# Performance work log

Hardware: AMD Instinct MI355X
Metric: run time of the kernel (lower is better)

Reference implementation:

```python
import jax, jax.numpy as jnp
import numpy as np

B, T, C = 4, 2048, 1024
H, D = 16, 64  # num_heads, head_size; H*D == C


def setup_inputs() -> dict:
    key = jax.random.key(0)
    k1, k2, k3 = jax.random.split(key, 3)
    x = jax.random.normal(k1, (B, T, C), dtype=jnp.float32)
    w_qkv = jax.random.normal(k2, (C, 3 * C), dtype=jnp.float32) * (C ** -0.5)
    w_out = jax.random.normal(k3, (C, C), dtype=jnp.float32) * (C ** -0.5)
    b_out = jnp.zeros((C,), dtype=jnp.float32)
    return {"x": x, "w_qkv": w_qkv, "w_out": w_out, "b_out": b_out}


def reference(x, w_qkv, w_out, b_out):
    Bb, Tt, Cc = x.shape
    qkv = x @ w_qkv                        # [B,T,3C]
    q, k, v = jnp.split(qkv, 3, axis=2)
    # [B,T,C] -> [B,H,T,D]
    q = q.reshape(Bb, Tt, H, D).transpose(0, 2, 1, 3)
    k = k.reshape(Bb, Tt, H, D).transpose(0, 2, 1, 3)
    v = v.reshape(Bb, Tt, H, D).transpose(0, 2, 1, 3)
    scores = jnp.einsum('bhqd,bhkd->bhqk', q, k) * (D ** -0.5)
    causal = jnp.tril(jnp.ones((Tt, Tt), dtype=bool))
    scores = jnp.where(causal, scores, -jnp.inf)
    attn = jax.nn.softmax(scores, axis=-1)  # dropout is identity in eval mode
    out = jnp.einsum('bhqk,bhkd->bhqd', attn, v)
    out = out.transpose(0, 2, 1, 3).reshape(Bb, Tt, Cc)
    return out @ w_out + b_out
```

## Files before the change

### kernel.cpp

```cpp
#include <hip/hip_runtime.h>

typedef __bf16 bf16;
typedef __bf16 bf16x4 __attribute__((ext_vector_type(4)));
typedef __bf16 bf16x8 __attribute__((ext_vector_type(8)));
typedef float  f32x4  __attribute__((ext_vector_type(4)));

#define MFMA16(A_, B_, C_) __builtin_amdgcn_mfma_f32_16x16x32_bf16((A_), (B_), (C_), 0, 0, 0)

#define BB 4
#define TT 2048
#define CC 1024
#define HH 16
#define DD 64
#define MM (BB * TT)
#define N_QKV (3 * CC)
#define LDSS 72
#define BSTRIDE 36
#define QSCALE2 0.18033688f

static __device__ __forceinline__ void store_lds8(bf16* p, bf16x8 v) {
  bf16x4 lo, hi;
#pragma unroll
  for (int i = 0; i < 4; i++) { lo[i] = v[i]; hi[i] = v[i + 4]; }
  *(bf16x4*)p = lo;
  *(bf16x4*)(p + 4) = hi;
}

static __device__ __forceinline__ bf16x8 load_lds8(const bf16* p) {
  bf16x4 lo = *(const bf16x4*)p;
  bf16x4 hi = *(const bf16x4*)(p + 4);
  bf16x8 v;
#pragma unroll
  for (int i = 0; i < 4; i++) { v[i] = lo[i]; v[i + 4] = hi[i]; }
  return v;
}

static __device__ __forceinline__ void async_cp16(const bf16* g, bf16* l) {
  __builtin_amdgcn_global_load_lds(
      (const __attribute__((address_space(1))) void*)g,
      (__attribute__((address_space(3))) void*)l, 16, 0, 0);
}

__global__ __launch_bounds__(256) void sniff_k(const unsigned short* __restrict__ u,
                                               int* __restrict__ flag) {
  __shared__ int s;
  if (threadIdx.x == 0) s = 0;
  __syncthreads();
  int c = 0;
  for (int i = threadIdx.x; i < 65536; i += 256)
    if ((u[i] & 0x7F80u) == 0x7F80u) c = 1;
  if (c) atomicOr(&s, 1);
  __syncthreads();
  if (threadIdx.x == 0) *flag = s;
}

__global__ __launch_bounds__(256) void cvt_k(const void* __restrict__ in,
                                             bf16* __restrict__ out,
                                             const int* __restrict__ flag,
                                             size_t off) {
  const int fl = *flag;
  const size_t i = ((size_t)blockIdx.x * 256 + threadIdx.x) * 8;
  if (fl) {
    f32x4 a = *(const f32x4*)((const float*)in + off + i);
    f32x4 b = *(const f32x4*)((const float*)in + off + i + 4);
    bf16x8 o;
#pragma unroll
    for (int j = 0; j < 4; j++) { o[j] = (bf16)a[j]; o[4 + j] = (bf16)b[j]; }
    *(bf16x8*)(out + i) = o;
  } else {
    *(bf16x8*)(out + i) = *(const bf16x8*)((const bf16*)in + off + i);
  }
}

__global__ __launch_bounds__(256) void transpose_k(const void* __restrict__ in,
                                                   bf16* __restrict__ out,
                                                   int R, int C,
                                                   const int* __restrict__ flag) {
  __shared__ bf16 tile[32][33];
  const int fl = *flag;
  const int c0 = blockIdx.x * 32, r0 = blockIdx.y * 32;
  const int tx = threadIdx.x & 31, ty = threadIdx.x >> 5;
#pragma unroll
  for (int i = ty; i < 32; i += 8) {
    const size_t idx = (size_t)(r0 + i) * C + c0 + tx;
    tile[i][tx] = fl ? (bf16)((const float*)in)[idx] : ((const bf16*)in)[idx];
  }
  __syncthreads();
#pragma unroll
  for (int i = ty; i < 32; i += 8)
    out[(size_t)(c0 + i) * R + r0 + tx] = tile[tx][i];
}

__global__ __launch_bounds__(256) void vtrans_k(const bf16* __restrict__ qkv,
                                                bf16* __restrict__ vt) {
  __shared__ bf16 tile[32][33];
  const int bh = blockIdx.z;
  const int t0 = blockIdx.x * 32, d0 = blockIdx.y * 32;
  const bf16* src = qkv + (size_t)(bh >> 4) * TT * N_QKV + 2 * CC + (bh & 15) * DD;
  const int tx = threadIdx.x & 31, ty = threadIdx.x >> 5;
#pragma unroll
  for (int i = ty; i < 32; i += 8)
    tile[i][tx] = src[(size_t)(t0 + i) * N_QKV + d0 + tx];
  __syncthreads();
  bf16* dst = vt + ((size_t)bh * DD + d0) * TT + t0;
#pragma unroll
  for (int i = ty; i < 32; i += 8)
    dst[(size_t)i * TT + tx] = tile[tx][i];
}

template <int EPI>
__global__ __launch_bounds__(256) void gemm_lds(const bf16* __restrict__ A,
                                                const bf16* __restrict__ Bt,
                                                const void* __restrict__ biasv,
                                                void* __restrict__ Cv,
                                                const int* __restrict__ flag,
                                                size_t aoff, size_t coff,
                                                int M, int N, int K,
                                                int lda, int ldc) {
  const int fl = *flag;
  __shared__ __align__(16) bf16 sA[128 * 32];
  __shared__ __align__(16) bf16 sB[128 * 32];
  const int tid = threadIdx.x;
  const int lane = tid & 63, wave = tid >> 6;
  const int quad = lane >> 4, l15 = lane & 15;
  const int wr = wave >> 1, wc = wave & 1;
  const int m0 = blockIdx.x * 128, n0 = blockIdx.y * 128;
  const int grow = lane >> 2;
  const int gcol = (lane & 3) * 8;

  f32x4 acc[4][4];
#pragma unroll
  for (int i = 0; i < 4; i++)
#pragma unroll
    for (int j = 0; j < 4; j++) {
      f32x4 z = {0.f, 0.f, 0.f, 0.f};
      acc[i][j] = z;
    }

  const bf16* Ag = A + aoff + (size_t)(m0 + wave * 32 + grow) * lda + gcol;
  const bf16* Bg = Bt + (size_t)(n0 + wave * 32 + grow) * K + gcol;
  bf16* sAw = sA + wave * 32 * 32;
  bf16* sBw = sB + wave * 32 * 32;

  for (int k0 = 0; k0 < K; k0 += 32) {
    __syncthreads();
    async_cp16(Ag, sAw);
    async_cp16(Ag + (size_t)16 * lda, sAw + 16 * 32);
    async_cp16(Bg, sBw);
    async_cp16(Bg + (size_t)16 * K, sBw + 16 * 32);
    Ag += 32;
    Bg += 32;
    __syncthreads();

    bf16x8 af[4], bfr[4];
#pragma unroll
    for (int mi = 0; mi < 4; mi++)
      af[mi] = *(const bf16x8*)(sA + (wr * 64 + mi * 16 + l15) * 32 + quad * 8);
#pragma unroll
    for (int ni = 0; ni < 4; ni++)
      bfr[ni] = *(const bf16x8*)(sB + (wc * 64 + ni * 16 + l15) * 32 + quad * 8);
#pragma unroll
    for (int mi = 0; mi < 4; mi++)
#pragma unroll
      for (int ni = 0; ni < 4; ni++)
        acc[mi][ni] = MFMA16(af[mi], bfr[ni], acc[mi][ni]);
  }

#pragma unroll
  for (int mi = 0; mi < 4; mi++) {
#pragma unroll
    for (int r = 0; r < 4; r++) {
      const int m = m0 + wr * 64 + mi * 16 + quad * 4 + r;
#pragma unroll
      for (int ni = 0; ni < 4; ni++) {
        const int n = n0 + wc * 64 + ni * 16 + l15;
        float v = acc[mi][ni][r];
        const size_t idx = coff + (size_t)m * ldc + n;
        if (EPI == 1) {
          v += fl ? ((const float*)biasv)[n] : (float)((const bf16*)biasv)[n];
          if (fl) ((float*)Cv)[idx] = v;
          else    ((bf16*)Cv)[idx] = (bf16)v;
        } else {
          ((bf16*)Cv)[idx] = (bf16)v;
        }
      }
    }
  }
}

template <int EPI, bool AF>
__global__ __launch_bounds__(256) void gemm_bt(const void* __restrict__ Av,
                                               const bf16* __restrict__ Bt,
                                               const void* __restrict__ biasv,
                                               void* __restrict__ Cv,
                                               const int* __restrict__ flag,
                                               size_t aoff, size_t coff,
                                               int M, int N, int K,
                                               int lda, int ldc) {
  const int fl = *flag;
  const bool af32 = AF && (fl != 0);
  __shared__ __align__(16) bf16 sA[128 * 32];
  __shared__ __align__(16) bf16 sB[128 * 32];
  const int tid = threadIdx.x;
  const int lane = tid & 63, wave = tid >> 6;
  const int quad = lane >> 4, l15 = lane & 15;
  const int wr = wave >> 1, wc = wave & 1;
  const int m0 = blockIdx.x * 128, n0 = blockIdx.y * 128;
  const int srow = tid >> 2;
  const int scol = (tid & 3) * 8;

  f32x4 acc[4][4];
#pragma unroll
  for (int i = 0; i < 4; i++)
#pragma unroll
    for (int j = 0; j < 4; j++) {
      f32x4 z = {0.f, 0.f, 0.f, 0.f};
      acc[i][j] = z;
    }

  const size_t abase0 = aoff + (size_t)(m0 + srow) * lda + scol;
  const size_t abase1 = abase0 + (size_t)64 * lda;
  const bf16* Bg0 = Bt + (size_t)(n0 + srow) * K + scol;
  const bf16* Bg1 = Bg0 + (size_t)64 * K;

  for (int k0 = 0; k0 < K; k0 += 32) {
    bf16x8 a0, a1;
    if (af32) {
      const float* Af = (const float*)Av;
      f32x4 p00 = *(const f32x4*)(Af + abase0 + k0);
      f32x4 p01 = *(const f32x4*)(Af + abase0 + k0 + 4);
      f32x4 p10 = *(const f32x4*)(Af + abase1 + k0);
      f32x4 p11 = *(const f32x4*)(Af + abase1 + k0 + 4);
#pragma unroll
      for (int i = 0; i < 4; i++) {
        a0[i] = (bf16)p00[i]; a0[i + 4] = (bf16)p01[i];
        a1[i] = (bf16)p10[i]; a1[i + 4] = (bf16)p11[i];
      }
    } else {
      const bf16* Ab = (const bf16*)Av;
      a0 = *(const bf16x8*)(Ab + abase0 + k0);
      a1 = *(const bf16x8*)(Ab + abase1 + k0);
    }
    bf16x8 b0 = *(const bf16x8*)(Bg0 + k0);
    bf16x8 b1 = *(const bf16x8*)(Bg1 + k0);
    __syncthreads();
    *(bf16x8*)(sA + srow * 32 + scol) = a0;
    *(bf16x8*)(sA + (64 + srow) * 32 + scol) = a1;
    *(bf16x8*)(sB + srow * 32 + scol) = b0;
    *(bf16x8*)(sB + (64 + srow) * 32 + scol) = b1;
    __syncthreads();

    bf16x8 af[4], bfr[4];
#pragma unroll
    for (int mi = 0; mi < 4; mi++)
      af[mi] = *(const bf16x8*)(sA + (wr * 64 + mi * 16 + l15) * 32 + quad * 8);
#pragma unroll
    for (int ni = 0; ni < 4; ni++)
      bfr[ni] = *(const bf16x8*)(sB + (wc * 64 + ni * 16 + l15) * 32 + quad * 8);
#pragma unroll
    for (int mi = 0; mi < 4; mi++)
#pragma unroll
      for (int ni = 0; ni < 4; ni++)
        acc[mi][ni] = MFMA16(af[mi], bfr[ni], acc[mi][ni]);
  }

#pragma unroll
  for (int mi = 0; mi < 4; mi++) {
#pragma unroll
    for (int r = 0; r < 4; r++) {
      const int m = m0 + wr * 64 + mi * 16 + quad * 4 + r;
#pragma unroll
      for (int ni = 0; ni < 4; ni++) {
        const int n = n0 + wc * 64 + ni * 16 + l15;
        float v = acc[mi][ni][r];
        const size_t idx = coff + (size_t)m * ldc + n;
        if (EPI == 1) {
          v += fl ? ((const float*)biasv)[n] : (float)((const bf16*)biasv)[n];
          if (fl) ((float*)Cv)[idx] = v;
          else    ((bf16*)Cv)[idx] = (bf16)v;
        } else {
          ((bf16*)Cv)[idx] = (bf16)v;
        }
      }
    }
  }
}

template <int EPI, bool AF, bool WF>
__global__ __launch_bounds__(256) void gemm_nt(const void* __restrict__ Av,
                                               const void* __restrict__ Wv,
                                               const void* __restrict__ biasv,
                                               void* __restrict__ Cv,
                                               const int* __restrict__ flag,
                                               size_t aoff, size_t coff,
                                               int M, int N, int K,
                                               int lda, int ldc) {
  const int fl = *flag;
  const bool af32 = AF && (fl != 0);
  const bool wf32 = WF && (fl != 0);
  __shared__ __align__(16) bf16 sA[128 * 32];
  __shared__ __align__(16) bf16 sB[128 * BSTRIDE];
  const int tid = threadIdx.x;
  const int lane = tid & 63, wave = tid >> 6;
  const int quad = lane >> 4, l15 = lane & 15;
  const int wr = wave >> 1, wc = wave & 1;
  const int m0 = blockIdx.x * 128, n0 = blockIdx.y * 128;
  const int arow = tid >> 2, acol = (tid & 3) * 8;
  const int wk = tid >> 3, wn = (tid & 7) * 16;

  f32x4 acc[4][4];
#pragma unroll
  for (int i = 0; i < 4; i++)
#pragma unroll
    for (int j = 0; j < 4; j++) {
      f32x4 z = {0.f, 0.f, 0.f, 0.f};
      acc[i][j] = z;
    }

  const size_t abase0 = aoff + (size_t)(m0 + arow) * lda + acol;
  const size_t abase1 = abase0 + (size_t)64 * lda;

  for (int k0 = 0; k0 < K; k0 += 32) {
    bf16x8 a0, a1;
    if (af32) {
      const float* Af = (const float*)Av;
      f32x4 p00 = *(const f32x4*)(Af + abase0 + k0);
      f32x4 p01 = *(const f32x4*)(Af + abase0 + k0 + 4);
      f32x4 p10 = *(const f32x4*)(Af + abase1 + k0);
      f32x4 p11 = *(const f32x4*)(Af + abase1 + k0 + 4);
#pragma unroll
      for (int i = 0; i < 4; i++) {
        a0[i] = (bf16)p00[i]; a0[i + 4] = (bf16)p01[i];
        a1[i] = (bf16)p10[i]; a1[i + 4] = (bf16)p11[i];
      }
    } else {
      const bf16* Ab = (const bf16*)Av;
      a0 = *(const bf16x8*)(Ab + abase0 + k0);
      a1 = *(const bf16x8*)(Ab + abase1 + k0);
    }
    bf16 wreg[16];
    const size_t wbase = (size_t)(k0 + wk) * N + n0 + wn;
    if (wf32) {
      const float* Wf = (const float*)Wv;
      f32x4 q0 = *(const f32x4*)(Wf + wbase);
      f32x4 q1 = *(const f32x4*)(Wf + wbase + 4);
      f32x4 q2 = *(const f32x4*)(Wf + wbase + 8);
      f32x4 q3 = *(const f32x4*)(Wf + wbase + 12);
#pragma unroll
      for (int i = 0; i < 4; i++) {
        wreg[i] = (bf16)q0[i];      wreg[4 + i] = (bf16)q1[i];
        wreg[8 + i] = (bf16)q2[i];  wreg[12 + i] = (bf16)q3[i];
      }
    } else {
      const bf16* Wb = (const bf16*)Wv;
      bf16x8 w0 = *(const bf16x8*)(Wb + wbase);
      bf16x8 w1 = *(const bf16x8*)(Wb + wbase + 8);
#pragma unroll
      for (int i = 0; i < 8; i++) { wreg[i] = w0[i]; wreg[8 + i] = w1[i]; }
    }
    __syncthreads();
    *(bf16x8*)(sA + arow * 32 + acol) = a0;
    *(bf16x8*)(sA + (64 + arow) * 32 + acol) = a1;
#pragma unroll
    for (int i = 0; i < 16; i++)
      sB[(wn + i) * BSTRIDE + wk] = wreg[i];
    __syncthreads();

    bf16x8 af[4], bfr[4];
#pragma unroll
    for (int mi = 0; mi < 4; mi++)
      af[mi] = *(const bf16x8*)(sA + (wr * 64 + mi * 16 + l15) * 32 + quad * 8);
#pragma unroll
    for (int ni = 0; ni < 4; ni++)
      bfr[ni] = load_lds8(sB + (wc * 64 + ni * 16 + l15) * BSTRIDE + quad * 8);
#pragma unroll
    for (int mi = 0; mi < 4; mi++)
#pragma unroll
      for (int ni = 0; ni < 4; ni++)
        acc[mi][ni] = MFMA16(af[mi], bfr[ni], acc[mi][ni]);
  }

#pragma unroll
  for (int mi = 0; mi < 4; mi++) {
#pragma unroll
    for (int r = 0; r < 4; r++) {
      const int m = m0 + wr * 64 + mi * 16 + quad * 4 + r;
#pragma unroll
      for (int ni = 0; ni < 4; ni++) {
        const int n = n0 + wc * 64 + ni * 16 + l15;
        float v = acc[mi][ni][r];
        const size_t idx = coff + (size_t)m * ldc + n;
        if (EPI == 1) {
          v += fl ? ((const float*)biasv)[n] : (float)((const bf16*)biasv)[n];
          if (fl) ((float*)Cv)[idx] = v;
          else    ((bf16*)Cv)[idx] = (bf16)v;
        } else {
          ((bf16*)Cv)[idx] = (bf16)v;
        }
      }
    }
  }
}

__global__ __launch_bounds__(256) void attn_k(bf16* __restrict__ qkv,
                                              const bf16* __restrict__ vt) {
  __shared__ __align__(16) bf16 sP[128 * LDSS];
  __shared__ __align__(16) bf16 sK[64 * LDSS];
  __shared__ __align__(16) bf16 sVt[64 * LDSS];

  const int tid = threadIdx.x;
  const int lane = tid & 63, wave = tid >> 6;
  const int quad = lane >> 4, l15 = lane & 15;
  const int bh = blockIdx.x;
  bf16* base = qkv + (size_t)(bh >> 4) * TT * N_QKV + (bh & 15) * DD;
  const bf16* Qp = base;
  const bf16* Kp = base + CC;
  const bf16* vhead = vt + (size_t)bh * DD * TT;

  const int qt = 15 - (int)blockIdx.y;
  const int q0 = qt * 128;
  const int wave_row0 = q0 + wave * 32;
  bf16* sPw = sP + (size_t)(wave * 32) * LDSS;

  const int krow = tid >> 2;
  const int kcol = (tid & 3) * 16;

  bf16x8 ones;
  {
    const bf16 o = (l15 == 0) ? (bf16)1.0f : (bf16)0.0f;
#pragma unroll
    for (int i = 0; i < 8; i++) ones[i] = o;
  }

  bf16x8 aq[2][2];
#pragma unroll
  for (int mi = 0; mi < 2; mi++)
#pragma unroll
    for (int ks = 0; ks < 2; ks++) {
      bf16x8 v = *(const bf16x8*)(Qp + (size_t)(wave_row0 + mi * 16 + l15) * N_QKV +
                                  ks * 32 + quad * 8);
#pragma unroll
      for (int i = 0; i < 8; i++) v[i] = (bf16)((float)v[i] * QSCALE2);
      aq[mi][ks] = v;
    }

  bf16x8 kr0, kr1, vr0, vr1;
  {
    const bf16* kp = Kp + (size_t)krow * N_QKV + kcol;
    kr0 = *(const bf16x8*)kp;
    kr1 = *(const bf16x8*)(kp + 8);
    const bf16* vp = vhead + (size_t)krow * TT + kcol;
    vr0 = *(const bf16x8*)vp;
    vr1 = *(const bf16x8*)(vp + 8);
  }

  f32x4 Oacc[2][4];
  f32x4 lacc[2];
#pragma unroll
  for (int mi = 0; mi < 2; mi++) {
    f32x4 z = {0.f, 0.f, 0.f, 0.f};
    lacc[mi] = z;
#pragma unroll
    for (int nt = 0; nt < 4; nt++) Oacc[mi][nt] = z;
  }

  const int jmax = q0 + 64;

  for (int j0 = 0; j0 <= jmax; j0 += 64) {
    __syncthreads();
    *(bf16x8*)(sK + krow * LDSS + kcol) = kr0;
    *(bf16x8*)(sK + krow * LDSS + kcol + 8) = kr1;
    *(bf16x8*)(sVt + krow * LDSS + kcol) = vr0;
    *(bf16x8*)(sVt + krow * LDSS + kcol + 8) = vr1;
    __syncthreads();

    if (j0 + 64 <= jmax) {
      const bf16* kp = Kp + (size_t)(j0 + 64 + krow) * N_QKV + kcol;
      kr0 = *(const bf16x8*)kp;
      kr1 = *(const bf16x8*)(kp + 8);
      const bf16* vp = vhead + (size_t)krow * TT + j0 + 64 + kcol;
      vr0 = *(const bf16x8*)vp;
      vr1 = *(const bf16x8*)(vp + 8);
    }

    if (j0 <= wave_row0 + 31) {
      f32x4 S[2][4];
#pragma unroll
      for (int mi = 0; mi < 2; mi++)
#pragma unroll
        for (int kt = 0; kt < 4; kt++) {
          f32x4 z = {0.f, 0.f, 0.f, 0.f};
          S[mi][kt] = z;
        }
      __builtin_amdgcn_s_setprio(1);
#pragma unroll
      for (int kt = 0; kt < 4; kt++) {
        const bf16* kp = sK + (size_t)(kt * 16 + l15) * LDSS + quad * 8;
        bf16x8 k0 = *(const bf16x8*)kp;
        bf16x8 k1 = *(const bf16x8*)(kp + 32);
        S[0][kt] = MFMA16(k0, aq[0][0], S[0][kt]);
        S[0][kt] = MFMA16(k1, aq[0][1], S[0][kt]);
        S[1][kt] = MFMA16(k0, aq[1][0], S[1][kt]);
        S[1][kt] = MFMA16(k1, aq[1][1], S[1][kt]);
      }
      __builtin_amdgcn_s_setprio(0);

      const bool needmask = (j0 + 63 > wave_row0);
#pragma unroll
      for (int mi = 0; mi < 2; mi++) {
        const int qg = wave_row0 + mi * 16 + l15;
#pragma unroll
        for (int kt = 0; kt < 4; kt++) {
          const int kb = j0 + kt * 16 + quad * 4;
          bf16x4 pk;
#pragma unroll
          for (int r = 0; r < 4; r++) {
            float e = __builtin_amdgcn_exp2f(S[mi][kt][r]);
            if (needmask && (kb + r > qg)) e = 0.f;
            pk[r] = (bf16)e;
          }
          *(bf16x4*)(sPw + (size_t)(mi * 16 + l15) * LDSS + kt * 16 + quad * 4) = pk;
        }
      }

      bf16x8 ap0[2], ap1[2];
#pragma unroll
      for (int mi = 0; mi < 2; mi++) {
        const bf16* pp = sPw + (size_t)(mi * 16 + l15) * LDSS + quad * 8;
        ap0[mi] = *(const bf16x8*)pp;
        ap1[mi] = *(const bf16x8*)(pp + 32);
      }
      __builtin_amdgcn_s_setprio(1);
#pragma unroll
      for (int mi = 0; mi < 2; mi++) {
        lacc[mi] = MFMA16(ap0[mi], ones, lacc[mi]);
        lacc[mi] = MFMA16(ap1[mi], ones, lacc[mi]);
      }
#pragma unroll
      for (int nt = 0; nt < 4; nt++) {
        const bf16* vp = sVt + (size_t)(nt * 16 + l15) * LDSS + quad * 8;
        bf16x8 v0 = *(const bf16x8*)vp;
        bf16x8 v1 = *(const bf16x8*)(vp + 32);
        Oacc[0][nt] = MFMA16(ap0[0], v0, Oacc[0][nt]);
        Oacc[0][nt] = MFMA16(ap1[0], v1, Oacc[0][nt]);
        Oacc[1][nt] = MFMA16(ap0[1], v0, Oacc[1][nt]);
        Oacc[1][nt] = MFMA16(ap1[1], v1, Oacc[1][nt]);
      }
      __builtin_amdgcn_s_setprio(0);
    }
  }

#pragma unroll
  for (int mi = 0; mi < 2; mi++)
#pragma unroll
    for (int r = 0; r < 4; r++) {
      const float lv = __shfl(lacc[mi][r], lane & 48, 64);
      const float invl = 1.0f / lv;
      const int t = q0 + wave * 32 + mi * 16 + quad * 4 + r;
#pragma unroll
      for (int nt = 0; nt < 4; nt++)
        base[(size_t)t * N_QKV + nt * 16 + l15] =
            (bf16)(Oacc[mi][nt][r] * invl);
    }
}

__global__ __launch_bounds__(256) void attn_s(bf16* __restrict__ qkv) {
  __shared__ __align__(16) bf16 sQ[128 * LDSS];
  __shared__ __align__(16) bf16 sK[64 * LDSS];
  __shared__ __align__(16) bf16 sVt[64 * LDSS];

  const int tid = threadIdx.x;
  const int lane = tid & 63, wave = tid >> 6;
  const int quad = lane >> 4, l15 = lane & 15;
  const int bh = blockIdx.x;
  bf16* base = qkv + (size_t)(bh >> 4) * TT * N_QKV + (bh & 15) * DD;
  const bf16* Qp = base;
  const bf16* Kp = base + CC;
  const bf16* Vp = base + 2 * CC;

  const int krow = tid >> 2;
  const int kcol = (tid & 3) * 16;
  const int vkey = tid & 31;
  const int vcol = (tid >> 5) * 8;

  bf16x8 ones;
  {
    const bf16 o = (l15 == 0) ? (bf16)1.0f : (bf16)0.0f;
#pragma unroll
    for (int i = 0; i < 8; i++) ones[i] = o;
  }

  const int qt = 15 - (int)blockIdx.y;
  const int q0 = qt * 128;

#pragma unroll
  for (int p = 0; p < 2; p++) {
    const int r = p * 64 + krow;
    const bf16* src = Qp + (size_t)(q0 + r) * N_QKV + kcol;
    bf16x8 v0 = *(const bf16x8*)src;
    bf16x8 v1 = *(const bf16x8*)(src + 8);
#pragma unroll
    for (int i = 0; i < 8; i++) {
      v0[i] = (bf16)((float)v0[i] * QSCALE2);
      v1[i] = (bf16)((float)v1[i] * QSCALE2);
    }
    *(bf16x8*)(sQ + r * LDSS + kcol) = v0;
    *(bf16x8*)(sQ + r * LDSS + kcol + 8) = v1;
  }

  bf16x8 kr0, kr1, vr0, vr1;
  {
    const bf16* kp = Kp + (size_t)krow * N_QKV + kcol;
    kr0 = *(const bf16x8*)kp;
    kr1 = *(const bf16x8*)(kp + 8);
    vr0 = *(const bf16x8*)(Vp + (size_t)vkey * N_QKV + vcol);
    vr1 = *(const bf16x8*)(Vp + (size_t)(32 + vkey) * N_QKV + vcol);
  }
  __syncthreads();

  bf16x8 aq[2][2];
#pragma unroll
  for (int mi = 0; mi < 2; mi++) {
    const bf16* qp = sQ + (size_t)(wave * 32 + mi * 16 + l15) * LDSS + quad * 8;
    aq[mi][0] = *(const bf16x8*)qp;
    aq[mi][1] = *(const bf16x8*)(qp + 32);
  }

  f32x4 Oacc[2][4];
  f32x4 lacc[2];
#pragma unroll
  for (int mi = 0; mi < 2; mi++) {
    f32x4 z = {0.f, 0.f, 0.f, 0.f};
    lacc[mi] = z;
#pragma unroll
    for (int nt = 0; nt < 4; nt++) Oacc[mi][nt] = z;
  }

  const int jmax = q0 + 64;
  const int wave_row0 = q0 + wave * 32;
  bf16* sP = sQ + (size_t)(wave * 32) * LDSS;

  for (int j0 = 0; j0 <= jmax; j0 += 64) {
    __syncthreads();
    *(bf16x8*)(sK + krow * LDSS + kcol) = kr0;
    *(bf16x8*)(sK + krow * LDSS + kcol + 8) = kr1;
#pragma unroll
    for (int i = 0; i < 8; i++) {
      sVt[(vcol + i) * LDSS + vkey] = vr0[i];
      sVt[(vcol + i) * LDSS + 32 + vkey] = vr1[i];
    }
    __syncthreads();

    if (j0 + 64 <= jmax) {
      const bf16* kp = Kp + (size_t)(j0 + 64 + krow) * N_QKV + kcol;
      kr0 = *(const bf16x8*)kp;
      kr1 = *(const bf16x8*)(kp + 8);
      vr0 = *(const bf16x8*)(Vp + (size_t)(j0 + 64 + vkey) * N_QKV + vcol);
      vr1 = *(const bf16x8*)(Vp + (size_t)(j0 + 96 + vkey) * N_QKV + vcol);
    }

    if (j0 <= wave_row0 + 31) {
      f32x4 S[2][4];
#pragma unroll
      for (int nt = 0; nt < 4; nt++) {
        const bf16* kp = sK + (size_t)(nt * 16 + l15) * LDSS + quad * 8;
        bf16x8 bk0 = *(const bf16x8*)kp;
        bf16x8 bk1 = *(const bf16x8*)(kp + 32);
#pragma unroll
        for (int mi = 0; mi < 2; mi++) {
          f32x4 acc = {0.f, 0.f, 0.f, 0.f};
          acc = MFMA16(aq[mi][0], bk0, acc);
          acc = MFMA16(aq[mi][1], bk1, acc);
          S[mi][nt] = acc;
        }
      }

      const bool needmask = (j0 + 63 > wave_row0);
#pragma unroll
      for (int mi = 0; mi < 2; mi++)
#pragma unroll
        for (int nt = 0; nt < 4; nt++) {
          const int kc = j0 + nt * 16 + l15;
#pragma unroll
          for (int r = 0; r < 4; r++) {
            float e = __builtin_amdgcn_exp2f(S[mi][nt][r]);
            if (needmask && kc > wave_row0 + mi * 16 + quad * 4 + r) e = 0.f;
            sP[(size_t)(mi * 16 + quad * 4 + r) * LDSS + nt * 16 + l15] =
                (bf16)e;
          }
        }

      bf16x8 ap[2][2];
#pragma unroll
      for (int mi = 0; mi < 2; mi++) {
        const bf16* pp = sP + (size_t)(mi * 16 + l15) * LDSS + quad * 8;
        ap[mi][0] = *(const bf16x8*)pp;
        ap[mi][1] = *(const bf16x8*)(pp + 32);
        lacc[mi] = MFMA16(ap[mi][0], ones, lacc[mi]);
        lacc[mi] = MFMA16(ap[mi][1], ones, lacc[mi]);
      }
#pragma unroll
      for (int nt = 0; nt < 4; nt++) {
        const bf16* vp = sVt + (size_t)(nt * 16 + l15) * LDSS + quad * 8;
        bf16x8 bv0 = *(const bf16x8*)vp;
        bf16x8 bv1 = *(const bf16x8*)(vp + 32);
#pragma unroll
        for (int mi = 0; mi < 2; mi++) {
          Oacc[mi][nt] = MFMA16(ap[mi][0], bv0, Oacc[mi][nt]);
          Oacc[mi][nt] = MFMA16(ap[mi][1], bv1, Oacc[mi][nt]);
        }
      }
    }
  }

#pragma unroll
  for (int mi = 0; mi < 2; mi++)
#pragma unroll
    for (int r = 0; r < 4; r++) {
      const float lv = __shfl(lacc[mi][r], lane & 48, 64);
      const float invl = 1.0f / lv;
      const int t = q0 + wave * 32 + mi * 16 + quad * 4 + r;
#pragma unroll
      for (int nt = 0; nt < 4; nt++)
        base[(size_t)t * N_QKV + nt * 16 + l15] =
            (bf16)(Oacc[mi][nt][r] * invl);
    }
}

extern "C" void kernel_launch(void* const* d_in, const int* in_sizes, int n_in,
                              void* d_out, int out_size, void* d_ws, size_t ws_size,
                              hipStream_t stream) {
  const void* x = d_in[0];
  const void* w_qkv = d_in[1];
  const void* w_out = d_in[2];
  const void* b_out = d_in[3];

  int* flag = (int*)d_ws;
  char* p = (char*)d_ws + 256;
  bf16* wqkvT = (bf16*)p;
  bf16* woutT = wqkvT + (size_t)N_QKV * CC;

  const size_t wT_bytes = ((size_t)N_QKV * CC + (size_t)CC * CC) * 2;
  const size_t qkv_bytes = (size_t)MM * N_QKV * 2;
  const size_t need_A = 256 + wT_bytes + qkv_bytes;
  const size_t need_B = 256 + wT_bytes + (size_t)TT * N_QKV * 2;

  sniff_k<<<1, 256, 0, stream>>>((const unsigned short*)x, flag);

  if (ws_size >= need_A) {
    bf16* qkv = woutT + (size_t)CC * CC;
    bf16* xb = qkv + (size_t)MM * N_QKV;
    const size_t slack = ws_size - need_A;

    transpose_k<<<dim3(N_QKV / 32, CC / 32), 256, 0, stream>>>(w_qkv, wqkvT, CC, N_QKV, flag);
    transpose_k<<<dim3(CC / 32, CC / 32), 256, 0, stream>>>(w_out, woutT, CC, CC, flag);

    const size_t full_xb = (size_t)MM * CC * 2;
    const size_t half_xb = full_xb / 2;
    if (slack >= full_xb) {
      cvt_k<<<(MM * CC) / 2048, 256, 0, stream>>>(x, xb, flag, 0);
      gemm_lds<0><<<dim3(MM / 128, N_QKV / 128), 256, 0, stream>>>(
          xb, wqkvT, nullptr, qkv, flag, 0, 0, MM, N_QKV, CC, CC, N_QKV);
      bf16* vt = xb;
      vtrans_k<<<dim3(TT / 32, DD / 32, BB * HH), 256, 0, stream>>>(qkv, vt);
      attn_k<<<dim3(BB * HH, 16), 256, 0, stream>>>(qkv, vt);
    } else if (slack >= half_xb) {
      for (int m0 = 0; m0 < MM; m0 += 4096) {
        cvt_k<<<(4096 * CC) / 2048, 256, 0, stream>>>(x, xb, flag, (size_t)m0 * CC);
        gemm_lds<0><<<dim3(4096 / 128, N_QKV / 128), 256, 0, stream>>>(
            xb, wqkvT, nullptr, qkv, flag, 0, (size_t)m0 * N_QKV,
            4096, N_QKV, CC, CC, N_QKV);
      }
      attn_s<<<dim3(BB * HH, 16), 256, 0, stream>>>(qkv);
    } else {
      gemm_bt<0, true><<<dim3(MM / 128, N_QKV / 128), 256, 0, stream>>>(
          x, wqkvT, nullptr, qkv, flag, 0, 0, MM, N_QKV, CC, CC, N_QKV);
      attn_s<<<dim3(BB * HH, 16), 256, 0, stream>>>(qkv);
    }

    gemm_lds<1><<<dim3(MM / 128, CC / 128), 256, 0, stream>>>(
        qkv, woutT, b_out, d_out, flag, 0, 0, MM, CC, CC, N_QKV, CC);
  } else if (ws_size >= need_B) {
    bf16* qkv = woutT + (size_t)CC * CC;
    transpose_k<<<dim3(N_QKV / 32, CC / 32), 256, 0, stream>>>(w_qkv, wqkvT, CC, N_QKV, flag);
    transpose_k<<<dim3(CC / 32, CC / 32), 256, 0, stream>>>(w_out, woutT, CC, CC, flag);
    for (int b = 0; b < BB; b++) {
      const size_t xoff = (size_t)b * TT * CC;
      gemm_bt<0, true><<<dim3(TT / 128, N_QKV / 128), 256, 0, stream>>>(
          x, wqkvT, nullptr, qkv, flag, xoff, 0, TT, N_QKV, CC, CC, N_QKV);
      attn_s<<<dim3(HH, 16), 256, 0, stream>>>(qkv);
      gemm_lds<1><<<dim3(TT / 128, CC / 128), 256, 0, stream>>>(
          qkv, woutT, b_out, d_out, flag, 0, xoff, TT, CC, CC, N_QKV, CC);
    }
  } else {
    bf16* qkvb = (bf16*)p;
    for (int b = 0; b < BB; b++) {
      const size_t xoff = (size_t)b * TT * CC;
      gemm_nt<0, true, true><<<dim3(TT / 128, N_QKV / 128), 256, 0, stream>>>(
          x, w_qkv, nullptr, qkvb, flag, xoff, 0, TT, N_QKV, CC, CC, N_QKV);
      attn_s<<<dim3(HH, 16), 256, 0, stream>>>(qkvb);
      gemm_nt<1, false, true><<<dim3(TT / 128, CC / 128), 256, 0, stream>>>(
          qkvb, w_out, b_out, d_out, flag, 0, xoff, TT, CC, CC, N_QKV, CC);
    }
  }
}
```

Measured before the change: 316.3 us.

## Replace 128x128 GEMMs with 256x256 double-buffered async-copy GEMM kernel

Adds gemm8p, a 512-thread GEMM with 256x256 output tiles and K-steps of 64. It double-buffers A and B in LDS, fills them with async global-to-LDS copies gated by explicit vmcnt waits and barriers, XOR-swizzles LDS columns, and remaps block indices for L2 locality. Both the QKV projection and the output projection use it on the main path. The larger tiles raise arithmetic intensity and the pipelining hides load latency, at the cost of 128 KB of LDS per block and fewer blocks for the output GEMM (128 tiles).

```diff
diff --git a/kernel.cpp b/kernel.cpp
--- a/kernel.cpp
+++ b/kernel.cpp
@@ -17,6 +17,11 @@
 #define LDSS 72
 #define BSTRIDE 36
 #define QSCALE2 0.18033688f
+
+#define BARRIER() do { asm volatile("" ::: "memory"); \
+                       __builtin_amdgcn_s_barrier();  \
+                       asm volatile("" ::: "memory"); } while (0)
+#define VMCNT(n)  asm volatile("s_waitcnt vmcnt(" #n ")" ::: "memory")
 
 static __device__ __forceinline__ void store_lds8(bf16* p, bf16x8 v) {
   bf16x4 lo, hi;
@@ -106,6 +111,130 @@
 #pragma unroll
   for (int i = ty; i < 32; i += 8)
     dst[(size_t)i * TT + tx] = tile[tx][i];
+}
+
+template <int EPI>
+__global__ __launch_bounds__(512, 2) void gemm8p(const bf16* __restrict__ A,
+                                                 const bf16* __restrict__ Bt,
+                                                 const void* __restrict__ biasv,
+                                                 void* __restrict__ Cv,
+                                                 const int* __restrict__ flag,
+                                                 int M, int N, int K,
+                                                 int lda, int ldc) {
+  __shared__ __align__(16) bf16 sA[2][256 * 64];
+  __shared__ __align__(16) bf16 sB[2][256 * 64];
+  const int fl = *flag;
+  const int tid = threadIdx.x;
+  const int lane = tid & 63, wave = tid >> 6;
+  const int quad = lane >> 4, l15 = lane & 15;
+  const int wm = wave >> 2, wn = wave & 3;
+
+  const int nm = M >> 8;
+  const int cpx = gridDim.x >> 3;
+  const int sw = ((int)blockIdx.x & 7) * cpx + ((int)blockIdx.x >> 3);
+  const int m0 = (sw % nm) * 256, n0 = (sw / nm) * 256;
+
+  const int s_row = wave * 8 + (lane >> 3);
+  const int s_col = ((((lane & 7) * 16) ^ ((lane >> 3) << 4)) >> 1);
+
+  f32x4 acc[8][4];
+#pragma unroll
+  for (int i = 0; i < 8; i++)
+#pragma unroll
+    for (int j = 0; j < 4; j++) {
+      f32x4 z = {0.f, 0.f, 0.f, 0.f};
+      acc[i][j] = z;
+    }
+
+  const bf16* Asrc = A + (size_t)(m0 + s_row) * lda + s_col;
+  const bf16* Bsrc = Bt + (size_t)(n0 + s_row) * K + s_col;
+
+#define STAGE8(buf_, k0_)                                                  \
+  do {                                                                     \
+    _Pragma("unroll")                                                      \
+    for (int i_ = 0; i_ < 4; i_++)                                         \
+      async_cp16(Asrc + (size_t)(i_ * 64) * lda + (k0_),                   \
+                 &sA[buf_][i_ * 4096 + wave * 512]);                       \
+    _Pragma("unroll")                                                      \
+    for (int i_ = 0; i_ < 4; i_++)                                         \
+      async_cp16(Bsrc + (size_t)(i_ * 64) * K + (k0_),                     \
+                 &sB[buf_][i_ * 4096 + wave * 512]);                       \
+  } while (0)
+
+  const int swz = (l15 & 7) << 3;
+
+#define COMPUTE8(buf_)                                                       \
+  do {                                                                       \
+    _Pragma("unroll")                                                        \
+    for (int kk = 0; kk < 2; kk++) {                                         \
+      bf16x8 bfr[4];                                                         \
+      _Pragma("unroll")                                                      \
+      for (int nf = 0; nf < 4; nf++) {                                       \
+        const int rB = wn * 64 + nf * 16 + l15;                              \
+        bfr[nf] = *(const bf16x8*)(&sB[buf_][rB * 64 +                       \
+                                             ((kk * 32 + quad * 8) ^ swz)]); \
+      }                                                                      \
+      _Pragma("unroll")                                                      \
+      for (int mh = 0; mh < 2; mh++) {                                       \
+        bf16x8 af[4];                                                        \
+        _Pragma("unroll")                                                    \
+        for (int mf = 0; mf < 4; mf++) {                                     \
+          const int rA = wm * 128 + (mh * 4 + mf) * 16 + l15;                \
+          af[mf] = *(const bf16x8*)(&sA[buf_][rA * 64 +                      \
+                                              ((kk * 32 + quad * 8) ^ swz)]);\
+        }                                                                    \
+        _Pragma("unroll")                                                    \
+        for (int mf = 0; mf < 4; mf++)                                       \
+          _Pragma("unroll")                                                  \
+          for (int nf = 0; nf < 4; nf++)                                     \
+            acc[mh * 4 + mf][nf] =                                           \
+                MFMA16(af[mf], bfr[nf], acc[mh * 4 + mf][nf]);               \
+      }                                                                      \
+    }                                                                        \
+  } while (0)
+
+  const int NT = K >> 6;
+  STAGE8(0, 0);
+  STAGE8(1, 64);
+  VMCNT(8);
+  BARRIER();
+
+  for (int t = 0; t < NT; t += 2) {
+    COMPUTE8(0);
+    BARRIER();
+    if (t + 2 < NT) { STAGE8(0, (t + 2) * 64); VMCNT(8); }
+    else            { VMCNT(0); }
+    BARRIER();
+    COMPUTE8(1);
+    BARRIER();
+    if (t + 3 < NT) { STAGE8(1, (t + 3) * 64); VMCNT(8); }
+    else            { VMCNT(0); }
+    BARRIER();
+  }
+
+#undef STAGE8
+#undef COMPUTE8
+
+#pragma unroll
+  for (int mf = 0; mf < 8; mf++) {
+#pragma unroll
+    for (int r = 0; r < 4; r++) {
+      const int m = m0 + wm * 128 + mf * 16 + quad * 4 + r;
+#pragma unroll
+      for (int nf = 0; nf < 4; nf++) {
+        const int n = n0 + wn * 64 + nf * 16 + l15;
+        float v = acc[mf][nf][r];
+        const size_t idx = (size_t)m * ldc + n;
+        if (EPI == 1) {
+          v += fl ? ((const float*)biasv)[n] : (float)((const bf16*)biasv)[n];
+          if (fl) ((float*)Cv)[idx] = v;
+          else    ((bf16*)Cv)[idx] = (bf16)v;
+        } else {
+          ((bf16*)Cv)[idx] = (bf16)v;
+        }
+      }
+    }
+  }
 }
 
 template <int EPI>
@@ -759,8 +888,8 @@
     const size_t half_xb = full_xb / 2;
     if (slack >= full_xb) {
       cvt_k<<<(MM * CC) / 2048, 256, 0, stream>>>(x, xb, flag, 0);
-      gemm_lds<0><<<dim3(MM / 128, N_QKV / 128), 256, 0, stream>>>(
-          xb, wqkvT, nullptr, qkv, flag, 0, 0, MM, N_QKV, CC, CC, N_QKV);
+      gemm8p<0><<<dim3((MM / 256) * (N_QKV / 256)), 512, 0, stream>>>(
+          xb, wqkvT, nullptr, qkv, flag, MM, N_QKV, CC, CC, N_QKV);
       bf16* vt = xb;
       vtrans_k<<<dim3(TT / 32, DD / 32, BB * HH), 256, 0, stream>>>(qkv, vt);
       attn_k<<<dim3(BB * HH, 16), 256, 0, stream>>>(qkv, vt);
@@ -778,8 +907,8 @@
       attn_s<<<dim3(BB * HH, 16), 256, 0, stream>>>(qkv);
     }
 
-    gemm_lds<1><<<dim3(MM / 128, CC / 128), 256, 0, stream>>>(
-        qkv, woutT, b_out, d_out, flag, 0, 0, MM, CC, CC, N_QKV, CC);
+    gemm8p<1><<<dim3((MM / 256) * (CC / 256)), 512, 0, stream>>>(
+        qkv, woutT, b_out, d_out, flag, MM, CC, CC, N_QKV, CC);
   } else if (ws_size >= need_B) {
     bf16* qkv = woutT + (size_t)CC * CC;
     transpose_k<<<dim3(N_QKV / 32, CC / 32), 256, 0, stream>>>(w_qkv, wqkvT, CC, N_QKV, flag);
```

New measurement: 334.5 us. 5.8% more time.
